# Kernel optimization log

Measured on AMD Instinct MI355X. Metric: run time of the kernel, lower is better.

## Reference

```python
import jax, jax.numpy as jnp
import numpy as np

B, T, DIM, HID, NE = 2, 512, 512, 2048, 64  # batch, seq, d_model, d_ff, n_experts


def setup_inputs() -> dict:
    key = jax.random.key(0)
    ks = jax.random.split(key, 7)
    s1, s2 = 1.0 / np.sqrt(DIM), 1.0 / np.sqrt(HID)
    return {
        "x": jax.random.normal(ks[0], (B, T, DIM), dtype=jnp.float32),
        "emb1": jax.random.normal(ks[1], (NE, DIM), dtype=jnp.float32) * s1,
        "W1": jax.random.normal(ks[2], (NE, DIM, HID), dtype=jnp.float32) * s1,
        "b1": jnp.zeros((NE, HID), dtype=jnp.float32),
        "emb2": jax.random.normal(ks[3], (NE, HID), dtype=jnp.float32) * s2,
        "W2": jax.random.normal(ks[4], (NE, HID, DIM), dtype=jnp.float32) * s2,
        "b2": jnp.zeros((NE, DIM), dtype=jnp.float32),
    }


def _moe_fc_tokens(x, emb, W, b):
    # x: [N, din]; emb: [E, din]; W: [E, din, dout]; b: [E, dout]
    din = x.shape[-1]
    logits = (x @ emb.T) / jnp.sqrt(jnp.asarray(din, x.dtype))  # [N, E]
    probs = jax.nn.softmax(logits, axis=-1)
    gate = jnp.max(probs, axis=-1)          # [N] top-1 gate value
    idx = jnp.argmax(probs, axis=-1)        # [N] top-1 expert id
    h = jnp.einsum('ni,eio->neo', x, W) + b[None]  # [N, E, dout]
    sel = jnp.take_along_axis(h, idx[:, None, None], axis=1)[:, 0]  # [N, dout]
    return sel * gate[:, None]


def reference(x, emb1, W1, b1, emb2, W2, b2):
    n = x.shape[0] * x.shape[1]
    xt = x.reshape(n, x.shape[-1])                  # [N, dim]
    h = _moe_fc_tokens(xt, emb1, W1, b1)            # [N, hid]
    h = jax.nn.gelu(h, approximate=False)           # nn.GELU default (erf)
    # dropout p=0.0 -> identity
    out = _moe_fc_tokens(h, emb2, W2, b2)           # [N, dim]
    return out.reshape(x.shape)
```

## Files before the change

### kernel.cpp

```cpp
#include <hip/hip_runtime.h>
#include <math.h>

constexpr int N    = 1024;
constexpr int DIM  = 512;
constexpr int HID  = 2048;
constexpr int NE   = 64;

__device__ inline void fma4(float4& a, float s, const float4& w) {
    a.x = fmaf(s, w.x, a.x);
    a.y = fmaf(s, w.y, a.y);
    a.z = fmaf(s, w.z, a.z);
    a.w = fmaf(s, w.w, a.w);
}

template <int DIN>
__global__ __launch_bounds__(256) void gating_kernel(
    const float* __restrict__ X, const float* __restrict__ emb,
    float* __restrict__ gate, int* __restrict__ idx, int* __restrict__ cnt)
{
    constexpr int TPB = 4;
    const int n0  = blockIdx.x * TPB;
    const int tid = threadIdx.x;

    __shared__ float  xs[TPB][DIN];
    __shared__ double red[256];

    for (int i = tid; i < TPB * (DIN / 4); i += 256) {
        const int tk = i / (DIN / 4), j = i % (DIN / 4);
        ((float4*)xs[tk])[j] = ((const float4*)(X + (size_t)(n0 + tk) * DIN))[j];
    }
    __syncthreads();

    const int e    = tid >> 2;
    const int part = tid & 3;
    constexpr int SEG = DIN / 4;

    const float4* w4 = (const float4*)(emb + (size_t)e * DIN + part * SEG);
    double acc[TPB] = {0.0, 0.0, 0.0, 0.0};

    for (int i = 0; i < SEG / 4; i++) {
        const float4 wv = w4[i];
        #pragma unroll
        for (int tk = 0; tk < TPB; tk++) {
            const float4 xv = ((const float4*)(xs[tk] + part * SEG))[i];
            acc[tk] += (double)xv.x * (double)wv.x + (double)xv.y * (double)wv.y
                     + (double)xv.z * (double)wv.z + (double)xv.w * (double)wv.w;
        }
    }

    for (int tk = 0; tk < TPB; tk++) {
        red[tid] = acc[tk];
        __syncthreads();
        if (tid < 64) {
            double s = red[tid * 4] + red[tid * 4 + 1] + red[tid * 4 + 2] + red[tid * 4 + 3];
            float  l = (float)(s / sqrt((double)DIN));

            float m = l; int mi = tid;
            #pragma unroll
            for (int off = 32; off > 0; off >>= 1) {
                float om = __shfl_down(m, off);
                int   oi = __shfl_down(mi, off);
                if (om > m || (om == m && oi < mi)) { m = om; mi = oi; }
            }
            m  = __shfl(m, 0);
            mi = __shfl(mi, 0);

            float p = expf(l - m);
            float ss = p;
            #pragma unroll
            for (int off = 32; off > 0; off >>= 1) ss += __shfl_down(ss, off);

            if (tid == 0) {
                gate[n0 + tk] = 1.0f / ss;
                idx[n0 + tk]  = mi;
                atomicAdd(&cnt[mi], 1);
            }
        }
        __syncthreads();
    }
}

__global__ __launch_bounds__(1024) void scan_scatter(
    const int* __restrict__ cnt, const int* __restrict__ idx,
    int* __restrict__ off, int* __restrict__ bucket)
{
    __shared__ int soff[NE];
    __shared__ int scur[NE];
    const int tid = threadIdx.x;

    if (tid == 0) {
        int s = 0;
        for (int e = 0; e < NE; e++) { soff[e] = s; off[e] = s; s += cnt[e]; }
    }
    if (tid < NE) scur[tid] = 0;
    __syncthreads();

    const int e = idx[tid];
    const int p = atomicAdd(&scur[e], 1);
    bucket[soff[e] + p] = tid;
}

__global__ __launch_bounds__(256, 2) void moe_gemm1(
    const float* __restrict__ X,  const float* __restrict__ W1,
    const float* __restrict__ b1, const float* __restrict__ gate,
    const int* __restrict__ cnt,  const int* __restrict__ off,
    const int* __restrict__ bucket, float* __restrict__ H)
{
    const int e    = blockIdx.x;
    const int mt   = cnt[e];
    if (mt == 0) return;
    const int base = off[e];
    const int tid  = threadIdx.x;
    const int tg   = tid >> 6;
    const int c    = blockIdx.y * 256 + (tid & 63) * 4;

    __shared__ float xs[32][DIM];

    const float* Wc = W1 + (size_t)e * DIM * HID + c;
    const float4 bias4 = *(const float4*)(b1 + (size_t)e * HID + c);

    for (int chunk = 0; chunk < mt; chunk += 32) {
        const int m = min(32, mt - chunk);

        for (int i = tid; i < m * (DIM / 4); i += 256) {
            const int t = i >> 7, j = i & 127;
            ((float4*)xs[t])[j] =
                ((const float4*)(X + (size_t)bucket[base + chunk + t] * DIM))[j];
        }
        __syncthreads();

        float4 acc[8];
        #pragma unroll
        for (int t = 0; t < 8; t++) acc[t] = make_float4(0.f, 0.f, 0.f, 0.f);

        float4 wr[4];
        #pragma unroll
        for (int r = 0; r < 4; r++)
            wr[r] = *(const float4*)(Wc + (size_t)r * HID);

        for (int dg = 0; dg < DIM / 4; dg++) {
            float4 wn[4];
            const bool more = (dg + 1 < DIM / 4);
            if (more) {
                const float* wq = Wc + (size_t)(dg + 1) * 4 * HID;
                #pragma unroll
                for (int r = 0; r < 4; r++)
                    wn[r] = *(const float4*)(wq + (size_t)r * HID);
            }
            #pragma unroll
            for (int t = 0; t < 8; t++) {
                const float4 xv = *(const float4*)&xs[tg * 8 + t][dg * 4];
                fma4(acc[t], xv.x, wr[0]);
                fma4(acc[t], xv.y, wr[1]);
                fma4(acc[t], xv.z, wr[2]);
                fma4(acc[t], xv.w, wr[3]);
            }
            if (more) {
                #pragma unroll
                for (int r = 0; r < 4; r++) wr[r] = wn[r];
            }
        }

        #pragma unroll
        for (int t = 0; t < 8; t++) {
            const int ti = chunk + tg * 8 + t;
            if (ti < mt) {
                const int   tok = bucket[base + ti];
                const float g   = gate[tok];
                float4 v;
                v.x = g * (acc[t].x + bias4.x);
                v.y = g * (acc[t].y + bias4.y);
                v.z = g * (acc[t].z + bias4.z);
                v.w = g * (acc[t].w + bias4.w);
                v.x = 0.5f * v.x * (1.0f + erff(v.x * 0.70710678118654752f));
                v.y = 0.5f * v.y * (1.0f + erff(v.y * 0.70710678118654752f));
                v.z = 0.5f * v.z * (1.0f + erff(v.z * 0.70710678118654752f));
                v.w = 0.5f * v.w * (1.0f + erff(v.w * 0.70710678118654752f));
                *(float4*)(H + (size_t)tok * HID + c) = v;
            }
        }
        __syncthreads();
    }
}

__global__ __launch_bounds__(256, 2) void moe_gemm2(
    const float* __restrict__ Hm, const float* __restrict__ W2,
    const float* __restrict__ b2, const float* __restrict__ gate,
    const int* __restrict__ cnt,  const int* __restrict__ off,
    const int* __restrict__ bucket, float* __restrict__ out)
{
    const int e    = blockIdx.x;
    const int z    = blockIdx.z;
    const int mt   = cnt[e];
    if (mt == 0) return;
    const int base = off[e];
    const int tid  = threadIdx.x;
    const int tg   = tid >> 6;
    const int c    = blockIdx.y * 256 + (tid & 63) * 4;

    __shared__ float xs[32][512];

    const float* Wc = W2 + (size_t)e * HID * DIM + (size_t)z * 512 * DIM + c;
    float4 bias4 = make_float4(0.f, 0.f, 0.f, 0.f);
    if (z == 0) bias4 = *(const float4*)(b2 + (size_t)e * DIM + c);

    for (int chunk = 0; chunk < mt; chunk += 32) {
        const int m = min(32, mt - chunk);

        for (int i = tid; i < m * 128; i += 256) {
            const int t = i >> 7, j = i & 127;
            ((float4*)xs[t])[j] =
                ((const float4*)(Hm + (size_t)bucket[base + chunk + t] * HID + z * 512))[j];
        }
        __syncthreads();

        float4 acc[8];
        #pragma unroll
        for (int t = 0; t < 8; t++) acc[t] = make_float4(0.f, 0.f, 0.f, 0.f);

        float4 wr[4];
        #pragma unroll
        for (int r = 0; r < 4; r++)
            wr[r] = *(const float4*)(Wc + (size_t)r * DIM);

        for (int dg = 0; dg < 128; dg++) {
            float4 wn[4];
            const bool more = (dg + 1 < 128);
            if (more) {
                const float* wq = Wc + (size_t)(dg + 1) * 4 * DIM;
                #pragma unroll
                for (int r = 0; r < 4; r++)
                    wn[r] = *(const float4*)(wq + (size_t)r * DIM);
            }
            #pragma unroll
            for (int t = 0; t < 8; t++) {
                const float4 xv = *(const float4*)&xs[tg * 8 + t][dg * 4];
                fma4(acc[t], xv.x, wr[0]);
                fma4(acc[t], xv.y, wr[1]);
                fma4(acc[t], xv.z, wr[2]);
                fma4(acc[t], xv.w, wr[3]);
            }
            if (more) {
                #pragma unroll
                for (int r = 0; r < 4; r++) wr[r] = wn[r];
            }
        }

        #pragma unroll
        for (int t = 0; t < 8; t++) {
            const int ti = chunk + tg * 8 + t;
            if (ti < mt) {
                const int   tok = bucket[base + ti];
                const float g   = gate[tok];
                float* o = out + (size_t)tok * DIM + c;
                atomicAdd(o + 0, g * (acc[t].x + bias4.x));
                atomicAdd(o + 1, g * (acc[t].y + bias4.y));
                atomicAdd(o + 2, g * (acc[t].z + bias4.z));
                atomicAdd(o + 3, g * (acc[t].w + bias4.w));
            }
        }
        __syncthreads();
    }
}

extern "C" void kernel_launch(void* const* d_in, const int* in_sizes, int n_in,
                              void* d_out, int out_size, void* d_ws, size_t ws_size,
                              hipStream_t stream)
{
    const float* x    = (const float*)d_in[0];
    const float* emb1 = (const float*)d_in[1];
    const float* W1   = (const float*)d_in[2];
    const float* b1   = (const float*)d_in[3];
    const float* emb2 = (const float*)d_in[4];
    const float* W2   = (const float*)d_in[5];
    const float* b2   = (const float*)d_in[6];
    float* out = (float*)d_out;

    float* H       = (float*)d_ws;
    float* gate1   = H + (size_t)N * HID;
    float* gate2   = gate1 + N;
    int*   idx1    = (int*)(gate2 + N);
    int*   idx2    = idx1 + N;
    int*   bucket1 = idx2 + N;
    int*   bucket2 = bucket1 + N;
    int*   cnt1    = bucket2 + N;
    int*   off1    = cnt1 + NE;
    int*   cnt2    = off1 + NE;
    int*   off2    = cnt2 + NE;

    hipMemsetAsync(cnt1, 0, 4 * NE * sizeof(int), stream);
    hipMemsetAsync(out, 0, (size_t)N * DIM * sizeof(float), stream);

    gating_kernel<DIM><<<N / 4, 256, 0, stream>>>(x, emb1, gate1, idx1, cnt1);
    scan_scatter<<<1, N, 0, stream>>>(cnt1, idx1, off1, bucket1);
    moe_gemm1<<<dim3(NE, HID / 256), 256, 0, stream>>>(x, W1, b1, gate1, cnt1, off1,
                                                       bucket1, H);
    gating_kernel<HID><<<N / 4, 256, 0, stream>>>(H, emb2, gate2, idx2, cnt2);
    scan_scatter<<<1, N, 0, stream>>>(cnt2, idx2, off2, bucket2);
    moe_gemm2<<<dim3(NE, DIM / 256, 4), 256, 0, stream>>>(H, W2, b2, gate2, cnt2, off2,
                                                          bucket2, out);
}
```

Measured before the change: 656.9 us.

## Double-buffer weight registers in expert GEMMs and raise split-K for second GEMM

Result: slower. 1.039 ms (+58.1%).

```diff
diff --git a/kernel.cpp b/kernel.cpp
--- a/kernel.cpp
+++ b/kernel.cpp
@@ -122,7 +122,7 @@
     for (int chunk = 0; chunk < mt; chunk += 32) {
         const int m = min(32, mt - chunk);
 
-        for (int i = tid; i < m * (DIM / 4); i += 256) {
+        for (int i = tid; i < m * 128; i += 256) {
             const int t = i >> 7, j = i & 127;
             ((float4*)xs[t])[j] =
                 ((const float4*)(X + (size_t)bucket[base + chunk + t] * DIM))[j];
@@ -133,31 +133,38 @@
         #pragma unroll
         for (int t = 0; t < 8; t++) acc[t] = make_float4(0.f, 0.f, 0.f, 0.f);
 
-        float4 wr[4];
-        #pragma unroll
-        for (int r = 0; r < 4; r++)
-            wr[r] = *(const float4*)(Wc + (size_t)r * HID);
-
-        for (int dg = 0; dg < DIM / 4; dg++) {
-            float4 wn[4];
-            const bool more = (dg + 1 < DIM / 4);
-            if (more) {
-                const float* wq = Wc + (size_t)(dg + 1) * 4 * HID;
-                #pragma unroll
-                for (int r = 0; r < 4; r++)
-                    wn[r] = *(const float4*)(wq + (size_t)r * HID);
-            }
+        float4 wA[4], wB[4];
+        #pragma unroll
+        for (int r = 0; r < 4; r++) wA[r] = *(const float4*)(Wc + (size_t)r * HID);
+        #pragma unroll
+        for (int r = 0; r < 4; r++) wB[r] = *(const float4*)(Wc + (size_t)(4 + r) * HID);
+
+        for (int dg = 0; dg < 128; dg += 2) {
             #pragma unroll
             for (int t = 0; t < 8; t++) {
                 const float4 xv = *(const float4*)&xs[tg * 8 + t][dg * 4];
-                fma4(acc[t], xv.x, wr[0]);
-                fma4(acc[t], xv.y, wr[1]);
-                fma4(acc[t], xv.z, wr[2]);
-                fma4(acc[t], xv.w, wr[3]);
-            }
-            if (more) {
+                fma4(acc[t], xv.x, wA[0]);
+                fma4(acc[t], xv.y, wA[1]);
+                fma4(acc[t], xv.z, wA[2]);
+                fma4(acc[t], xv.w, wA[3]);
+            }
+            if (dg + 2 < 128) {
+                const float* wq = Wc + (size_t)(dg + 2) * 4 * HID;
                 #pragma unroll
-                for (int r = 0; r < 4; r++) wr[r] = wn[r];
+                for (int r = 0; r < 4; r++) wA[r] = *(const float4*)(wq + (size_t)r * HID);
+            }
+            #pragma unroll
+            for (int t = 0; t < 8; t++) {
+                const float4 xv = *(const float4*)&xs[tg * 8 + t][dg * 4 + 4];
+                fma4(acc[t], xv.x, wB[0]);
+                fma4(acc[t], xv.y, wB[1]);
+                fma4(acc[t], xv.z, wB[2]);
+                fma4(acc[t], xv.w, wB[3]);
+            }
+            if (dg + 3 < 128) {
+                const float* wq = Wc + (size_t)(dg + 3) * 4 * HID;
+                #pragma unroll
+                for (int r = 0; r < 4; r++) wB[r] = *(const float4*)(wq + (size_t)r * HID);
             }
         }
 
@@ -183,7 +190,7 @@
     }
 }
 
-__global__ __launch_bounds__(256, 2) void moe_gemm2(
+__global__ __launch_bounds__(256, 4) void moe_gemm2(
     const float* __restrict__ Hm, const float* __restrict__ W2,
     const float* __restrict__ b2, const float* __restrict__ gate,
     const int* __restrict__ cnt,  const int* __restrict__ off,
@@ -198,19 +205,19 @@
     const int tg   = tid >> 6;
     const int c    = blockIdx.y * 256 + (tid & 63) * 4;
 
-    __shared__ float xs[32][512];
-
-    const float* Wc = W2 + (size_t)e * HID * DIM + (size_t)z * 512 * DIM + c;
+    __shared__ float xs[32][256];
+
+    const float* Wc = W2 + (size_t)e * HID * DIM + (size_t)z * 256 * DIM + c;
     float4 bias4 = make_float4(0.f, 0.f, 0.f, 0.f);
     if (z == 0) bias4 = *(const float4*)(b2 + (size_t)e * DIM + c);
 
     for (int chunk = 0; chunk < mt; chunk += 32) {
         const int m = min(32, mt - chunk);
 
-        for (int i = tid; i < m * 128; i += 256) {
-            const int t = i >> 7, j = i & 127;
+        for (int i = tid; i < m * 64; i += 256) {
+            const int t = i >> 6, j = i & 63;
             ((float4*)xs[t])[j] =
-                ((const float4*)(Hm + (size_t)bucket[base + chunk + t] * HID + z * 512))[j];
+                ((const float4*)(Hm + (size_t)bucket[base + chunk + t] * HID + z * 256))[j];
         }
         __syncthreads();
 
@@ -218,31 +225,38 @@
         #pragma unroll
         for (int t = 0; t < 8; t++) acc[t] = make_float4(0.f, 0.f, 0.f, 0.f);
 
-        float4 wr[4];
-        #pragma unroll
-        for (int r = 0; r < 4; r++)
-            wr[r] = *(const float4*)(Wc + (size_t)r * DIM);
-
-        for (int dg = 0; dg < 128; dg++) {
-            float4 wn[4];
-            const bool more = (dg + 1 < 128);
-            if (more) {
-                const float* wq = Wc + (size_t)(dg + 1) * 4 * DIM;
-                #pragma unroll
-                for (int r = 0; r < 4; r++)
-                    wn[r] = *(const float4*)(wq + (size_t)r * DIM);
-            }
+        float4 wA[4], wB[4];
+        #pragma unroll
+        for (int r = 0; r < 4; r++) wA[r] = *(const float4*)(Wc + (size_t)r * DIM);
+        #pragma unroll
+        for (int r = 0; r < 4; r++) wB[r] = *(const float4*)(Wc + (size_t)(4 + r) * DIM);
+
+        for (int dg = 0; dg < 64; dg += 2) {
             #pragma unroll
             for (int t = 0; t < 8; t++) {
                 const float4 xv = *(const float4*)&xs[tg * 8 + t][dg * 4];
-                fma4(acc[t], xv.x, wr[0]);
-                fma4(acc[t], xv.y, wr[1]);
-                fma4(acc[t], xv.z, wr[2]);
-                fma4(acc[t], xv.w, wr[3]);
-            }
-            if (more) {
+                fma4(acc[t], xv.x, wA[0]);
+                fma4(acc[t], xv.y, wA[1]);
+                fma4(acc[t], xv.z, wA[2]);
+                fma4(acc[t], xv.w, wA[3]);
+            }
+            if (dg + 2 < 64) {
+                const float* wq = Wc + (size_t)(dg + 2) * 4 * DIM;
                 #pragma unroll
-                for (int r = 0; r < 4; r++) wr[r] = wn[r];
+                for (int r = 0; r < 4; r++) wA[r] = *(const float4*)(wq + (size_t)r * DIM);
+            }
+            #pragma unroll
+            for (int t = 0; t < 8; t++) {
+                const float4 xv = *(const float4*)&xs[tg * 8 + t][dg * 4 + 4];
+                fma4(acc[t], xv.x, wB[0]);
+                fma4(acc[t], xv.y, wB[1]);
+                fma4(acc[t], xv.z, wB[2]);
+                fma4(acc[t], xv.w, wB[3]);
+            }
+            if (dg + 3 < 64) {
+                const float* wq = Wc + (size_t)(dg + 3) * 4 * DIM;
+                #pragma unroll
+                for (int r = 0; r < 4; r++) wB[r] = *(const float4*)(wq + (size_t)r * DIM);
             }
         }
 
@@ -297,6 +311,6 @@
                                                        bucket1, H);
     gating_kernel<HID><<<N / 4, 256, 0, stream>>>(H, emb2, gate2, idx2, cnt2);
     scan_scatter<<<1, N, 0, stream>>>(cnt2, idx2, off2, bucket2);
-    moe_gemm2<<<dim3(NE, DIM / 256, 4), 256, 0, stream>>>(H, W2, b2, gate2, cnt2, off2,
+    moe_gemm2<<<dim3(NE, DIM / 256, 8), 256, 0, stream>>>(H, W2, b2, gate2, cnt2, off2,
                                                           bucket2, out);
 }
```
